# Performance work log

Hardware: AMD Instinct MI355X
Metric: run time of the kernel (lower is better)

## Reference

```python
import jax, jax.numpy as jnp
import numpy as np

B, L, D = 2048, 200, 128
HID = [80, 40]


def setup_inputs() -> dict:
    key = jax.random.key(0)
    ks = jax.random.split(key, 10)
    hist_emb = jax.random.normal(ks[0], (B, L, D), dtype=jnp.float32)
    target_emb = jax.random.normal(ks[1], (B, D), dtype=jnp.float32)
    mask = jax.random.randint(ks[2], (B, L), 0, 2, dtype=jnp.int32)
    # MLP params: (4D -> 80 -> 40 -> 1), Kaiming-uniform-ish like nn.Linear default
    dims = [4 * D] + HID + [1]
    params = {}
    for i in range(len(dims) - 1):
        fan_in = dims[i]
        bound = 1.0 / np.sqrt(fan_in)
        params[f"W{i}"] = jax.random.uniform(ks[3 + 2 * i], (dims[i], dims[i + 1]), minval=-bound, maxval=bound, dtype=jnp.float32)
        params[f"b{i}"] = jax.random.uniform(ks[4 + 2 * i], (dims[i + 1],), minval=-bound, maxval=bound, dtype=jnp.float32)
    return {"hist_emb": hist_emb, "target_emb": target_emb, "mask": mask, **params}


def reference(hist_emb, target_emb, mask, W0, b0, W1, b1, W2, b2):
    # hist_emb: (B,L,D); target_emb: (B,D); mask: (B,L)
    target = target_emb[:, None, :]                       # (B,1,D) -> broadcast over L
    diff = hist_emb - target
    prod = hist_emb * target
    tgt = jnp.broadcast_to(target, hist_emb.shape)
    feat = jnp.concatenate([hist_emb, tgt, diff, prod], axis=-1)  # (B,L,4D)
    h = jax.nn.relu(jnp.einsum("blf,fh->blh", feat, W0) + b0)
    h = jax.nn.relu(jnp.einsum("blf,fh->blh", h, W1) + b1)
    scores = (jnp.einsum("blf,fh->blh", h, W2) + b2)[..., 0]      # (B,L)
    m = mask.astype(scores.dtype)
    logits = scores + (1.0 - m) * -1e9
    attn = jax.nn.softmax(logits, axis=1)                 # (B,L)
    user_interest = jnp.einsum("bl,bld->bd", attn, hist_emb)
    return user_interest, attn
```

## Files before the change

### kernel.cpp

```cpp
#include <hip/hip_runtime.h>
#include <hip/hip_bf16.h>

#define B_  2048
#define L_  200
#define D_  128
#define H0_ 80
#define H1_ 40
#define NTILE 13

#define WS_BG  0
#define WS_W1T 20480
#define WS_W0P 25088
#define WS_TOT 35840

typedef __attribute__((ext_vector_type(8))) short short8;
typedef __attribute__((ext_vector_type(4))) float floatx4;

__device__ __forceinline__ short f2bf(float f) {
    unsigned u = __float_as_uint(f);
    u += 0x7fffu + ((u >> 16) & 1u);
    return (short)(u >> 16);
}
__device__ __forceinline__ float bf2f(short s) {
    return __uint_as_float(((unsigned)(unsigned short)s) << 16);
}

__global__ __launch_bounds__(256) void prep_kernel(
    const float* __restrict__ W0, const float* __restrict__ W1,
    short* __restrict__ ws)
{
    for (int i = blockIdx.x * 256 + threadIdx.x; i < WS_TOT; i += 64 * 256) {
        short v;
        if (i < WS_W1T) {
            int h = i >> 8, k = i & 255;
            float x = (k < 128) ? (W0[(size_t)k * H0_ + h] + W0[(size_t)(256 + k) * H0_ + h])
                                : W0[(size_t)(384 + (k - 128)) * H0_ + h];
            v = f2bf(x);
        } else if (i < WS_W0P) {
            int j = i - WS_W1T;
            int n = j / 96, k = j - n * 96;
            v = (n < H1_ && k < H0_) ? f2bf(W1[(size_t)k * H1_ + n]) : (short)0;
        } else {
            int j = i - WS_W0P;
            int d = j / 84, h = j - d * 84;
            v = (h < H0_) ? f2bf(W0[(size_t)(128 + d) * H0_ + h] - W0[(size_t)(256 + d) * H0_ + h])
                          : (short)0;
        }
        ws[i] = v;
    }
}

__global__ __launch_bounds__(256, 2) void fused_kernel(
    const float* __restrict__ hist, const float* __restrict__ tgt,
    const int* __restrict__ mask, const short* __restrict__ ws,
    const float* __restrict__ b0p, const float* __restrict__ b1,
    const float* __restrict__ W2, const float* __restrict__ b2,
    float* __restrict__ out)
{
    __shared__ __align__(16) short wbuf[10560];
    __shared__ __align__(16) short h0t[4][16][100];
    __shared__ float tgs[D_];
    __shared__ float beffs[H0_];
    __shared__ float scores[208];
    __shared__ float red[8];

    const int tid = threadIdx.x;
    const int wave = tid >> 6, lane = tid & 63;
    const int col = lane & 15, quad = lane >> 4;
    const int b = blockIdx.x;

    if (tid < D_) tgs[tid] = tgt[(size_t)b * D_ + tid];
    if (tid < 128) {
        int w = tid >> 5, row = (tid >> 1) & 15, c = 80 + (tid & 1) * 8;
        *(short8*)&h0t[w][row][c] = (short8)0;
    }
    short8 w1f[3][3];
    #pragma unroll
    for (int ks = 0; ks < 3; ++ks)
        #pragma unroll
        for (int nt = 0; nt < 3; ++nt)
            w1f[ks][nt] = *(const short8*)(ws + WS_W1T + (nt * 16 + col) * 96 + ks * 32 + quad * 8);
    float b1r[3], w2r[3];
    #pragma unroll
    for (int nt = 0; nt < 3; ++nt) {
        int h = nt * 16 + col;
        b1r[nt] = (h < H1_) ? b1[h] : 0.f;
        w2r[nt] = (h < H1_) ? W2[h] : 0.f;
    }
    const float b2v = b2[0];
    __syncthreads();

    for (int i = tid; i < 1280; i += 256) {
        int h = i >> 4, d0 = (i & 15) * 8;
        short8 wa = *(const short8*)(ws + WS_BG + h * 256 + d0);
        short8 wd = *(const short8*)(ws + WS_BG + h * 256 + 128 + d0);
        floatx4 t0 = *(const floatx4*)&tgs[d0];
        floatx4 t1 = *(const floatx4*)&tgs[d0 + 4];
        short8 o;
        #pragma unroll
        for (int j = 0; j < 4; ++j) o[j] = f2bf(bf2f(wa[j]) + t0[j] * bf2f(wd[j]));
        #pragma unroll
        for (int j = 4; j < 8; ++j) o[j] = f2bf(bf2f(wa[j]) + t1[j - 4] * bf2f(wd[j]));
        *(short8*)(wbuf + h * 132 + d0) = o;
    }
    float* red2 = &scores[0];
    if (tid < 160) {
        int seg = tid / 80, h = tid - seg * 80;
        int d0 = seg * 64;
        float s = 0.f;
        #pragma unroll 8
        for (int d = d0; d < d0 + 64; ++d)
            s += tgs[d] * bf2f(ws[WS_W0P + d * 84 + h]);
        red2[seg * 80 + h] = s;
    }
    __syncthreads();
    if (tid < H0_) beffs[tid] = b0p[tid] + red2[tid] + red2[80 + tid];
    __syncthreads();

    float ber[5];
    #pragma unroll
    for (int nt = 0; nt < 5; ++nt) ber[nt] = beffs[nt * 16 + col];

    for (int t = wave; t < NTILE; t += 4) {
        const int l = t * 16 + col;
        const int lc = (l < L_) ? l : (L_ - 1);
        const float* ap = hist + ((size_t)b * L_ + lc) * D_ + quad * 8;

        floatx4 A[8];
        #pragma unroll
        for (int u = 0; u < 8; ++u)
            A[u] = *(const floatx4*)(ap + (u >> 1) * 32 + (u & 1) * 4);

        short8 ah[4];
        #pragma unroll
        for (int ks = 0; ks < 4; ++ks) {
            short8 h8;
            #pragma unroll
            for (int j = 0; j < 8; ++j) h8[j] = f2bf(A[2 * ks + (j >> 2)][j & 3]);
            ah[ks] = h8;
        }

        floatx4 c0[5];
        #pragma unroll
        for (int nt = 0; nt < 5; ++nt) c0[nt] = (floatx4)0.f;
        __builtin_amdgcn_s_setprio(1);
        #pragma unroll
        for (int ks = 0; ks < 4; ++ks)
            #pragma unroll
            for (int nt = 0; nt < 5; ++nt) {
                short8 bfr = *(const short8*)(wbuf + (nt * 16 + col) * 132 + ks * 32 + quad * 8);
                c0[nt] = __builtin_amdgcn_mfma_f32_16x16x32_bf16(ah[ks], bfr, c0[nt], 0, 0, 0);
            }
        __builtin_amdgcn_s_setprio(0);

        #pragma unroll
        for (int nt = 0; nt < 5; ++nt) {
            #pragma unroll
            for (int r = 0; r < 4; ++r) {
                float v = c0[nt][r] + ber[nt];
                v = v > 0.f ? v : 0.f;
                h0t[wave][quad * 4 + r][nt * 16 + col] = f2bf(v);
            }
        }

        floatx4 c1[3];
        #pragma unroll
        for (int nt = 0; nt < 3; ++nt) c1[nt] = (floatx4)0.f;
        __builtin_amdgcn_s_setprio(1);
        #pragma unroll
        for (int ks = 0; ks < 3; ++ks) {
            short8 a1 = *(const short8*)&h0t[wave][col][ks * 32 + quad * 8];
            #pragma unroll
            for (int nt = 0; nt < 3; ++nt)
                c1[nt] = __builtin_amdgcn_mfma_f32_16x16x32_bf16(a1, w1f[ks][nt], c1[nt], 0, 0, 0);
        }
        __builtin_amdgcn_s_setprio(0);

        float s4[4] = {0.f, 0.f, 0.f, 0.f};
        #pragma unroll
        for (int nt = 0; nt < 3; ++nt)
            #pragma unroll
            for (int r = 0; r < 4; ++r) {
                float v = c1[nt][r] + b1r[nt];
                v = v > 0.f ? v : 0.f;
                s4[r] += v * w2r[nt];
            }
        #pragma unroll
        for (int r = 0; r < 4; ++r) {
            s4[r] += __shfl_xor(s4[r], 1, 16);
            s4[r] += __shfl_xor(s4[r], 2, 16);
            s4[r] += __shfl_xor(s4[r], 4, 16);
            s4[r] += __shfl_xor(s4[r], 8, 16);
        }
        if (col == 0) {
            #pragma unroll
            for (int r = 0; r < 4; ++r)
                scores[t * 16 + quad * 4 + r] = s4[r] + b2v;
        }
    }
    __syncthreads();

    float sc = -3.0e38f;
    if (tid < L_) {
        sc = scores[tid];
        if (mask[(size_t)b * L_ + tid] == 0) sc -= 1e9f;
    }
    float m = sc;
    #pragma unroll
    for (int off = 32; off >= 1; off >>= 1) m = fmaxf(m, __shfl_xor(m, off, 64));
    if (lane == 0) red[wave] = m;
    __syncthreads();
    m = fmaxf(fmaxf(red[0], red[1]), fmaxf(red[2], red[3]));
    float e = (tid < L_) ? __expf(sc - m) : 0.f;
    float s = e;
    #pragma unroll
    for (int off = 32; off >= 1; off >>= 1) s += __shfl_xor(s, off, 64);
    if (lane == 0) red[4 + wave] = s;
    __syncthreads();
    s = red[4] + red[5] + red[6] + red[7];
    float av = e * (1.0f / s);
    if (tid < L_) {
        scores[tid] = av;
        out[(size_t)B_ * D_ + (size_t)b * L_ + tid] = av;
    }
    __syncthreads();

    float* pw = (float*)&h0t[0][0][0];
    {
        const int rsel = lane >> 5;
        const int d0 = (lane & 31) * 4;
        const int rbase = wave * 50;
        const float* hb = hist + ((size_t)b * L_ + rbase + rsel) * D_ + d0;
        floatx4 acc = (floatx4)0.f;
        #pragma unroll 25
        for (int i = 0; i < 25; ++i) {
            float w = scores[rbase + 2 * i + rsel];
            floatx4 h4 = *(const floatx4*)(hb + (size_t)(2 * i) * D_);
            acc.x = fmaf(w, h4.x, acc.x);
            acc.y = fmaf(w, h4.y, acc.y);
            acc.z = fmaf(w, h4.z, acc.z);
            acc.w = fmaf(w, h4.w, acc.w);
        }
        acc.x += __shfl_xor(acc.x, 32, 64);
        acc.y += __shfl_xor(acc.y, 32, 64);
        acc.z += __shfl_xor(acc.z, 32, 64);
        acc.w += __shfl_xor(acc.w, 32, 64);
        if (rsel == 0) *(floatx4*)&pw[wave * 128 + d0] = acc;
    }
    __syncthreads();
    if (tid < D_)
        out[(size_t)b * D_ + tid] = (pw[tid] + pw[128 + tid]) + (pw[256 + tid] + pw[384 + tid]);
}

extern "C" void kernel_launch(void* const* d_in, const int* in_sizes, int n_in,
                              void* d_out, int out_size, void* d_ws, size_t ws_size,
                              hipStream_t stream) {
    const float* hist = (const float*)d_in[0];
    const float* tgt  = (const float*)d_in[1];
    const int*   mask = (const int*)d_in[2];
    const float* W0   = (const float*)d_in[3];
    const float* b0   = (const float*)d_in[4];
    const float* W1   = (const float*)d_in[5];
    const float* b1   = (const float*)d_in[6];
    const float* W2   = (const float*)d_in[7];
    const float* b2   = (const float*)d_in[8];

    short* ws = (short*)d_ws;

    prep_kernel<<<64, 256, 0, stream>>>(W0, W1, ws);
    fused_kernel<<<B_, 256, 0, stream>>>(hist, tgt, mask, ws, b0, b1, W2, b2,
                                         (float*)d_out);
}
```

Measured before the change: 334.5 us.

## Drop weight prep kernel and build bf16 weights inside the fused kernel

Removes the separate prep launch that packed W0/W1 into bf16 workspace, and instead has every block read fp32 W0/W1 from global memory and convert them on the fly into shared memory and registers. It also removes the s_setprio hints around the MFMA loops. This saves one kernel launch and its dependency, but each of the 2048 blocks now reads more weight data, with scattered scalar loads for W1 and the W0 difference terms and strided 2-byte shared stores, so per-block prologue cost goes up.

```diff
diff --git a/kernel.cpp b/kernel.cpp
--- a/kernel.cpp
+++ b/kernel.cpp
@@ -8,11 +8,6 @@
 #define H1_ 40
 #define NTILE 13
 
-#define WS_BG  0
-#define WS_W1T 20480
-#define WS_W0P 25088
-#define WS_TOT 35840
-
 typedef __attribute__((ext_vector_type(8))) short short8;
 typedef __attribute__((ext_vector_type(4))) float floatx4;
 
@@ -25,37 +20,12 @@
     return __uint_as_float(((unsigned)(unsigned short)s) << 16);
 }
 
-__global__ __launch_bounds__(256) void prep_kernel(
-    const float* __restrict__ W0, const float* __restrict__ W1,
-    short* __restrict__ ws)
-{
-    for (int i = blockIdx.x * 256 + threadIdx.x; i < WS_TOT; i += 64 * 256) {
-        short v;
-        if (i < WS_W1T) {
-            int h = i >> 8, k = i & 255;
-            float x = (k < 128) ? (W0[(size_t)k * H0_ + h] + W0[(size_t)(256 + k) * H0_ + h])
-                                : W0[(size_t)(384 + (k - 128)) * H0_ + h];
-            v = f2bf(x);
-        } else if (i < WS_W0P) {
-            int j = i - WS_W1T;
-            int n = j / 96, k = j - n * 96;
-            v = (n < H1_ && k < H0_) ? f2bf(W1[(size_t)k * H1_ + n]) : (short)0;
-        } else {
-            int j = i - WS_W0P;
-            int d = j / 84, h = j - d * 84;
-            v = (h < H0_) ? f2bf(W0[(size_t)(128 + d) * H0_ + h] - W0[(size_t)(256 + d) * H0_ + h])
-                          : (short)0;
-        }
-        ws[i] = v;
-    }
-}
-
 __global__ __launch_bounds__(256, 2) void fused_kernel(
     const float* __restrict__ hist, const float* __restrict__ tgt,
-    const int* __restrict__ mask, const short* __restrict__ ws,
-    const float* __restrict__ b0p, const float* __restrict__ b1,
-    const float* __restrict__ W2, const float* __restrict__ b2,
-    float* __restrict__ out)
+    const int* __restrict__ mask, const float* __restrict__ W0,
+    const float* __restrict__ b0p, const float* __restrict__ W1,
+    const float* __restrict__ b1, const float* __restrict__ W2,
+    const float* __restrict__ b2, float* __restrict__ out)
 {
     __shared__ __align__(16) short wbuf[10560];
     __shared__ __align__(16) short h0t[4][16][100];
@@ -78,8 +48,16 @@
     #pragma unroll
     for (int ks = 0; ks < 3; ++ks)
         #pragma unroll
-        for (int nt = 0; nt < 3; ++nt)
-            w1f[ks][nt] = *(const short8*)(ws + WS_W1T + (nt * 16 + col) * 96 + ks * 32 + quad * 8);
+        for (int nt = 0; nt < 3; ++nt) {
+            const int n = nt * 16 + col;
+            short8 f;
+            #pragma unroll
+            for (int j = 0; j < 8; ++j) {
+                const int k = ks * 32 + quad * 8 + j;
+                f[j] = (n < H1_ && k < H0_) ? f2bf(W1[(size_t)k * H1_ + n]) : (short)0;
+            }
+            w1f[ks][nt] = f;
+        }
     float b1r[3], w2r[3];
     #pragma unroll
     for (int nt = 0; nt < 3; ++nt) {
@@ -91,17 +69,23 @@
     __syncthreads();
 
     for (int i = tid; i < 1280; i += 256) {
-        int h = i >> 4, d0 = (i & 15) * 8;
-        short8 wa = *(const short8*)(ws + WS_BG + h * 256 + d0);
-        short8 wd = *(const short8*)(ws + WS_BG + h * 256 + 128 + d0);
-        floatx4 t0 = *(const floatx4*)&tgs[d0];
-        floatx4 t1 = *(const floatx4*)&tgs[d0 + 4];
-        short8 o;
-        #pragma unroll
-        for (int j = 0; j < 4; ++j) o[j] = f2bf(bf2f(wa[j]) + t0[j] * bf2f(wd[j]));
-        #pragma unroll
-        for (int j = 4; j < 8; ++j) o[j] = f2bf(bf2f(wa[j]) + t1[j - 4] * bf2f(wd[j]));
-        *(short8*)(wbuf + h * 132 + d0) = o;
+        const int d = i / 10, hh = (i - d * 10) * 8;
+        const float t = tgs[d];
+        floatx4 a0 = *(const floatx4*)(W0 + (size_t)d * H0_ + hh);
+        floatx4 a1 = *(const floatx4*)(W0 + (size_t)d * H0_ + hh + 4);
+        floatx4 c0 = *(const floatx4*)(W0 + (size_t)(256 + d) * H0_ + hh);
+        floatx4 c1 = *(const floatx4*)(W0 + (size_t)(256 + d) * H0_ + hh + 4);
+        floatx4 p0 = *(const floatx4*)(W0 + (size_t)(384 + d) * H0_ + hh);
+        floatx4 p1 = *(const floatx4*)(W0 + (size_t)(384 + d) * H0_ + hh + 4);
+        #pragma unroll
+        for (int j = 0; j < 4; ++j) {
+            short wa = f2bf(a0[j] + c0[j]);
+            short wd = f2bf(p0[j]);
+            wbuf[(hh + j) * 132 + d] = f2bf(bf2f(wa) + t * bf2f(wd));
+            short wa2 = f2bf(a1[j] + c1[j]);
+            short wd2 = f2bf(p1[j]);
+            wbuf[(hh + 4 + j) * 132 + d] = f2bf(bf2f(wa2) + t * bf2f(wd2));
+        }
     }
     float* red2 = &scores[0];
     if (tid < 160) {
@@ -109,8 +93,10 @@
         int d0 = seg * 64;
         float s = 0.f;
         #pragma unroll 8
-        for (int d = d0; d < d0 + 64; ++d)
-            s += tgs[d] * bf2f(ws[WS_W0P + d * 84 + h]);
+        for (int d = d0; d < d0 + 64; ++d) {
+            short w = f2bf(W0[(size_t)(128 + d) * H0_ + h] - W0[(size_t)(256 + d) * H0_ + h]);
+            s += tgs[d] * bf2f(w);
+        }
         red2[seg * 80 + h] = s;
     }
     __syncthreads();
@@ -143,7 +129,6 @@
         floatx4 c0[5];
         #pragma unroll
         for (int nt = 0; nt < 5; ++nt) c0[nt] = (floatx4)0.f;
-        __builtin_amdgcn_s_setprio(1);
         #pragma unroll
         for (int ks = 0; ks < 4; ++ks)
             #pragma unroll
@@ -151,7 +136,6 @@
                 short8 bfr = *(const short8*)(wbuf + (nt * 16 + col) * 132 + ks * 32 + quad * 8);
                 c0[nt] = __builtin_amdgcn_mfma_f32_16x16x32_bf16(ah[ks], bfr, c0[nt], 0, 0, 0);
             }
-        __builtin_amdgcn_s_setprio(0);
 
         #pragma unroll
         for (int nt = 0; nt < 5; ++nt) {
@@ -166,7 +150,6 @@
         floatx4 c1[3];
         #pragma unroll
         for (int nt = 0; nt < 3; ++nt) c1[nt] = (floatx4)0.f;
-        __builtin_amdgcn_s_setprio(1);
         #pragma unroll
         for (int ks = 0; ks < 3; ++ks) {
             short8 a1 = *(const short8*)&h0t[wave][col][ks * 32 + quad * 8];
@@ -174,7 +157,6 @@
             for (int nt = 0; nt < 3; ++nt)
                 c1[nt] = __builtin_amdgcn_mfma_f32_16x16x32_bf16(a1, w1f[ks][nt], c1[nt], 0, 0, 0);
         }
-        __builtin_amdgcn_s_setprio(0);
 
         float s4[4] = {0.f, 0.f, 0.f, 0.f};
         #pragma unroll
@@ -265,9 +247,8 @@
     const float* W2   = (const float*)d_in[7];
     const float* b2   = (const float*)d_in[8];
 
-    short* ws = (short*)d_ws;
-
-    prep_kernel<<<64, 256, 0, stream>>>(W0, W1, ws);
-    fused_kernel<<<B_, 256, 0, stream>>>(hist, tgt, mask, ws, b0, b1, W2, b2,
+    (void)d_ws; (void)ws_size;
+
+    fused_kernel<<<B_, 256, 0, stream>>>(hist, tgt, mask, W0, b0, W1, b1, W2, b2,
                                          (float*)d_out);
 }
```

After: 360.3 us. +7.7%, slower.

## Fuse attention-weighted pooling into the MLP tile loop with online softmax

Applied to the files above, without the earlier changes.

Each wave now keeps a running max and a rescaled weighted sum of the hist rows it already holds in registers for the MLP. The final pooling becomes a cross-wave rescale-and-sum using the per-wave maxima, so the second global read of hist and an extra barrier phase are gone. The mask is also cached in shared memory, and the s_setprio hints around the MFMA blocks are dropped. In exchange each lane holds 32 more live accumulator floats (register pressure, possible occupancy loss), and each tile pays extra exp and shuffle work.

```diff
diff --git a/kernel.cpp b/kernel.cpp
--- a/kernel.cpp
+++ b/kernel.cpp
@@ -63,6 +63,8 @@
     __shared__ float beffs[H0_];
     __shared__ float scores[208];
     __shared__ float red[8];
+    __shared__ float mws[4];
+    __shared__ int   mks[200];
 
     const int tid = threadIdx.x;
     const int wave = tid >> 6, lane = tid & 63;
@@ -70,6 +72,7 @@
     const int b = blockIdx.x;
 
     if (tid < D_) tgs[tid] = tgt[(size_t)b * D_ + tid];
+    if (tid < 200) mks[tid] = mask[(size_t)b * L_ + tid];
     if (tid < 128) {
         int w = tid >> 5, row = (tid >> 1) & 15, c = 80 + (tid & 1) * 8;
         *(short8*)&h0t[w][row][c] = (short8)0;
@@ -121,6 +124,11 @@
     #pragma unroll
     for (int nt = 0; nt < 5; ++nt) ber[nt] = beffs[nt * 16 + col];
 
+    floatx4 acc8[8];
+    #pragma unroll
+    for (int u = 0; u < 8; ++u) acc8[u] = (floatx4)0.f;
+    float m_w = -3.0e38f;
+
     for (int t = wave; t < NTILE; t += 4) {
         const int l = t * 16 + col;
         const int lc = (l < L_) ? l : (L_ - 1);
@@ -143,7 +151,6 @@
         floatx4 c0[5];
         #pragma unroll
         for (int nt = 0; nt < 5; ++nt) c0[nt] = (floatx4)0.f;
-        __builtin_amdgcn_s_setprio(1);
         #pragma unroll
         for (int ks = 0; ks < 4; ++ks)
             #pragma unroll
@@ -151,7 +158,6 @@
                 short8 bfr = *(const short8*)(wbuf + (nt * 16 + col) * 132 + ks * 32 + quad * 8);
                 c0[nt] = __builtin_amdgcn_mfma_f32_16x16x32_bf16(ah[ks], bfr, c0[nt], 0, 0, 0);
             }
-        __builtin_amdgcn_s_setprio(0);
 
         #pragma unroll
         for (int nt = 0; nt < 5; ++nt) {
@@ -166,7 +172,6 @@
         floatx4 c1[3];
         #pragma unroll
         for (int nt = 0; nt < 3; ++nt) c1[nt] = (floatx4)0.f;
-        __builtin_amdgcn_s_setprio(1);
         #pragma unroll
         for (int ks = 0; ks < 3; ++ks) {
             short8 a1 = *(const short8*)&h0t[wave][col][ks * 32 + quad * 8];
@@ -174,7 +179,6 @@
             for (int nt = 0; nt < 3; ++nt)
                 c1[nt] = __builtin_amdgcn_mfma_f32_16x16x32_bf16(a1, w1f[ks][nt], c1[nt], 0, 0, 0);
         }
-        __builtin_amdgcn_s_setprio(0);
 
         float s4[4] = {0.f, 0.f, 0.f, 0.f};
         #pragma unroll
@@ -197,13 +201,48 @@
             for (int r = 0; r < 4; ++r)
                 scores[t * 16 + quad * 4 + r] = s4[r] + b2v;
         }
+
+        float sraw = scores[t * 16 + col];
+        float se = (l < L_) ? (mks[lc] ? sraw : sraw - 1e9f) : -3.0e38f;
+        float tm = se;
+        #pragma unroll
+        for (int off = 32; off >= 1; off >>= 1) tm = fmaxf(tm, __shfl_xor(tm, off, 64));
+        float mnew = fmaxf(m_w, tm);
+        float f = __expf(m_w - mnew);
+        float wexp = __expf(se - mnew);
+        #pragma unroll
+        for (int u = 0; u < 8; ++u) {
+            #pragma unroll
+            for (int j = 0; j < 4; ++j)
+                acc8[u][j] = acc8[u][j] * f + wexp * A[u][j];
+        }
+        m_w = mnew;
+    }
+
+    #pragma unroll
+    for (int u = 0; u < 8; ++u)
+        #pragma unroll
+        for (int j = 0; j < 4; ++j) {
+            acc8[u][j] += __shfl_xor(acc8[u][j], 1, 16);
+            acc8[u][j] += __shfl_xor(acc8[u][j], 2, 16);
+            acc8[u][j] += __shfl_xor(acc8[u][j], 4, 16);
+            acc8[u][j] += __shfl_xor(acc8[u][j], 8, 16);
+        }
+    {
+        float* pwv = (float*)&h0t[wave][0][0];
+        if (col == 0) {
+            #pragma unroll
+            for (int u = 0; u < 8; ++u)
+                *(floatx4*)&pwv[quad * 8 + (u >> 1) * 32 + (u & 1) * 4] = acc8[u];
+        }
+        if (lane == 0) mws[wave] = m_w;
     }
     __syncthreads();
 
     float sc = -3.0e38f;
     if (tid < L_) {
         sc = scores[tid];
-        if (mask[(size_t)b * L_ + tid] == 0) sc -= 1e9f;
+        if (mks[tid] == 0) sc -= 1e9f;
     }
     float m = sc;
     #pragma unroll
@@ -218,38 +257,19 @@
     if (lane == 0) red[4 + wave] = s;
     __syncthreads();
     s = red[4] + red[5] + red[6] + red[7];
-    float av = e * (1.0f / s);
-    if (tid < L_) {
-        scores[tid] = av;
-        out[(size_t)B_ * D_ + (size_t)b * L_ + tid] = av;
-    }
-    __syncthreads();
-
-    float* pw = (float*)&h0t[0][0][0];
-    {
-        const int rsel = lane >> 5;
-        const int d0 = (lane & 31) * 4;
-        const int rbase = wave * 50;
-        const float* hb = hist + ((size_t)b * L_ + rbase + rsel) * D_ + d0;
-        floatx4 acc = (floatx4)0.f;
-        #pragma unroll 25
-        for (int i = 0; i < 25; ++i) {
-            float w = scores[rbase + 2 * i + rsel];
-            floatx4 h4 = *(const floatx4*)(hb + (size_t)(2 * i) * D_);
-            acc.x = fmaf(w, h4.x, acc.x);
-            acc.y = fmaf(w, h4.y, acc.y);
-            acc.z = fmaf(w, h4.z, acc.z);
-            acc.w = fmaf(w, h4.w, acc.w);
-        }
-        acc.x += __shfl_xor(acc.x, 32, 64);
-        acc.y += __shfl_xor(acc.y, 32, 64);
-        acc.z += __shfl_xor(acc.z, 32, 64);
-        acc.w += __shfl_xor(acc.w, 32, 64);
-        if (rsel == 0) *(floatx4*)&pw[wave * 128 + d0] = acc;
-    }
-    __syncthreads();
-    if (tid < D_)
-        out[(size_t)b * D_ + tid] = (pw[tid] + pw[128 + tid]) + (pw[256 + tid] + pw[384 + tid]);
+    const float inv = 1.0f / s;
+    if (tid < L_)
+        out[(size_t)B_ * D_ + (size_t)b * L_ + tid] = e * inv;
+
+    if (tid < D_) {
+        float ui = 0.f;
+        #pragma unroll
+        for (int w2 = 0; w2 < 4; ++w2) {
+            const float* pwv = (const float*)&h0t[w2][0][0];
+            ui += pwv[tid] * __expf(mws[w2] - m);
+        }
+        out[(size_t)b * D_ + tid] = ui * inv;
+    }
 }
 
 extern "C" void kernel_launch(void* const* d_in, const int* in_sizes, int n_in,
```

Measured after the change: 330.9 us. No clear change (-1.1%).
